# Kernel tuning notes

Hardware: AMD Instinct MI355X
Metric: run time of the kernel (lower is better)

Reference implementation:

```python
import jax, jax.numpy as jnp
import numpy as np

N_Q, N_T, D, C = 4096, 8192, 512, 16
SIGMA = 2.0


def setup_inputs() -> dict:
    key = jax.random.key(0)
    k1, k2, k3 = jax.random.split(key, 3)
    X = jax.random.normal(k1, (N_Q, D), dtype=jnp.float32)
    X_train = jax.random.normal(k2, (N_T, D), dtype=jnp.float32)
    y = jax.random.randint(k3, (N_T,), 0, C, dtype=jnp.int32)
    sigma = jnp.float32(SIGMA)
    return {"X": X, "X_train": X_train, "y": y, "sigma": sigma}


def reference(X, X_train, y, sigma):
    xx = jnp.sum(X * X, axis=1, keepdims=True)              # [N_q, 1]
    tt = jnp.sum(X_train * X_train, axis=1)                 # [N_t]
    cross = jnp.einsum('qd,td->qt', X, X_train)             # [N_q, N_t]
    dist2 = jnp.maximum(xx + tt[None, :] - 2.0 * cross, 0.0)
    pattern = jnp.exp(-dist2 / (2.0 * sigma ** 2))          # Gaussian RBF kernel [N_q, N_t]
    # per-class segment sum over training patterns (replaces per-class Python loop)
    summation = jax.ops.segment_sum(pattern.T, y, num_segments=C).T  # [N_q, C]
    summation = summation / jnp.sum(summation, axis=1, keepdims=True)
    return jnp.argmax(summation, axis=1)
```

## Files before the change

kernel.cpp:

```cpp
#include <hip/hip_runtime.h>


#define NQ 4096
#define NT 8192
#define DD 512
#define NC 16
#define LN_FLT_MIN -87.336544750402f
#define SCREEN_T 750.0f

typedef __attribute__((ext_vector_type(4))) int   v4i;
typedef __attribute__((ext_vector_type(8))) int   v8i;
typedef __attribute__((ext_vector_type(16))) float f32x16;

static __device__ __forceinline__ unsigned f2fp4(float x) {
  const float a = __builtin_fabsf(x);
  unsigned i = (unsigned)(a >= 0.25f) + (a >= 0.75f) + (a >= 1.25f)
             + (a >= 1.75f) + (a >= 2.5f) + (a >= 3.5f) + (a >= 5.0f);
  return i | (x < 0.0f ? 8u : 0u);
}

__global__ __launch_bounds__(256) void prep_k(const float* __restrict__ X,
                                              const float* __restrict__ XT,
                                              unsigned char* __restrict__ fXp,
                                              unsigned char* __restrict__ fTp,
                                              float* __restrict__ xx,
                                              float* __restrict__ tt,
                                              float* __restrict__ classacc) {
  const int lane = threadIdx.x & 63;
  const int row  = blockIdx.x * 4 + (threadIdx.x >> 6);
  const float* src; unsigned char* dst; float* nrm; int r;
  if (row < NT) { r = row; src = XT + (size_t)r * DD; dst = fTp; nrm = tt + r; }
  else { r = row - NT; src = X + (size_t)r * DD; dst = fXp; nrm = xx + r; }
  const float4* s4 = (const float4*)src;
  const float4 a = s4[lane * 2], b = s4[lane * 2 + 1];
  const unsigned word =  f2fp4(a.x)        | (f2fp4(a.y) << 4)
                      | (f2fp4(a.z) << 8)  | (f2fp4(a.w) << 12)
                      | (f2fp4(b.x) << 16) | (f2fp4(b.y) << 20)
                      | (f2fp4(b.z) << 24) | (f2fp4(b.w) << 28);
  const int l = (r & 31) + 32 * ((lane >> 2) & 1);
  const size_t dest = ((size_t)(r >> 5) * 8 + (lane >> 3)) * 1024
                    + l * 16 + (lane & 3) * 4;
  *(unsigned*)(dst + dest) = word;
  float acc = a.x*a.x + a.y*a.y + a.z*a.z + a.w*a.w
            + b.x*b.x + b.y*b.y + b.z*b.z + b.w*b.w;
  #pragma unroll
  for (int off = 32; off; off >>= 1) acc += __shfl_down(acc, off, 64);
  if (lane == 0) *nrm = acc;
  if (blockIdx.x < 64) {
    float4 z = {0.f, 0.f, 0.f, 0.f};
    ((float4*)classacc)[blockIdx.x * 256 + threadIdx.x] = z;
  }
}

#define MFMA4(A, B, C) __builtin_amdgcn_mfma_scale_f32_32x32x64_f8f6f4( \
    (A), (B), (C), 4, 4, 0, 127, 0, 127)
#define BAR() __builtin_amdgcn_s_barrier()
#define WAITV0() asm volatile("s_waitcnt vmcnt(0)" ::: "memory")
#define WAITLGKM0() asm volatile("s_waitcnt lgkmcnt(0)" ::: "memory")

static __device__ __forceinline__ void gll(const unsigned char* src, char* dst) {
  __builtin_amdgcn_global_load_lds(
      (const __attribute__((address_space(1))) unsigned int*)src,
      (__attribute__((address_space(3))) unsigned int*)dst, 16, 0, 0);
}

static __device__ __forceinline__ v8i pk8(v4i lo) {
  return __builtin_shufflevector(lo, lo, 0, 1, 2, 3, -1, -1, -1, -1);
}

__global__ __launch_bounds__(512, 1) void pnn_mfma(const unsigned char* __restrict__ fXp,
                                                   const unsigned char* __restrict__ fTp,
                                                   const float* __restrict__ Xf,
                                                   const float* __restrict__ Tf,
                                                   const int* __restrict__ y,
                                                   const float* __restrict__ sigp,
                                                   const float* __restrict__ xx,
                                                   const float* __restrict__ tt,
                                                   float* __restrict__ classacc) {
  extern __shared__ char lds[];
  float* const hxs = (float*)(lds + 131072);
  const int tid  = threadIdx.x;
  const int w    = tid >> 6, lane = tid & 63;
  const int la   = lane & 31, lb = lane >> 5;
  const int wr   = w >> 2, wc = w & 3;

  const int bid   = blockIdx.x;
  const int strip = bid & 7;
  const int qt    = bid >> 3;
  const int qbase = qt * 128;
  const int rt0   = (qbase >> 5) + wr * 2;

  const float sg = sigp[0];
  const float inv2s2 = 1.0f / (2.0f * sg * sg);

  v4i av[2][8];
  #pragma unroll
  for (int mt = 0; mt < 2; ++mt)
    #pragma unroll
    for (int kt = 0; kt < 8; ++kt)
      av[mt][kt] = *(const v4i*)(fXp + ((size_t)(rt0 + mt) * 8 + kt) * 1024 + lane * 16);

  if (tid < 128) hxs[tid] = (xx[qbase + tid] - SCREEN_T) * 0.5f;

#define STAGEB(buf, trt0) { \
    _Pragma("unroll") \
    for (int j = 0; j < 8; ++j) \
      gll(fTp + ((size_t)((trt0) + j) * 8 + w) * 1024 + lane * 16, \
          (buf) + (j * 8 + w) * 1024 + lane * 16); }

  char* cur = lds;
  char* nxt = lds + 65536;

  STAGEB(cur, strip * 32)
  WAITV0();
  WAITLGKM0();
  BAR();

  #pragma clang loop unroll(disable)
  for (int t = 0; t < 4; ++t) {
    if (t < 3) STAGEB(nxt, strip * 32 + (t + 1) * 8)

    f32x16 acc00 = (f32x16)(0.f), acc01 = (f32x16)(0.f);
    f32x16 acc10 = (f32x16)(0.f), acc11 = (f32x16)(0.f);

    #pragma unroll
    for (int kt = 0; kt < 8; ++kt) {
      const v4i b0 = *(const v4i*)(cur + ((wc * 2 + 0) * 8 + kt) * 1024 + lane * 16);
      const v4i b1 = *(const v4i*)(cur + ((wc * 2 + 1) * 8 + kt) * 1024 + lane * 16);
      const v8i a0 = pk8(av[0][kt]), a1 = pk8(av[1][kt]);
      const v8i bb0 = pk8(b0), bb1 = pk8(b1);
      acc00 = MFMA4(a0, bb0, acc00);
      acc01 = MFMA4(a0, bb1, acc01);
      acc10 = MFMA4(a1, bb0, acc10);
      acc11 = MFMA4(a1, bb1, acc11);
    }

    const int tbase = strip * 1024 + t * 256;
    const int wt = tbase + wc * 64;
    const float h0 = tt[wt + la] * 0.5f;
    const float h1 = tt[wt + 32 + la] * 0.5f;

#define EPIL(ACC, mt, HN, nt) { \
    _Pragma("unroll") \
    for (int reg = 0; reg < 16; ++reg) { \
      const int ql = wr * 64 + (mt) * 32 + (reg & 3) + 8 * (reg >> 2) + 4 * lb; \
      if (__builtin_expect((ACC)[reg] > hxs[ql] + (HN), 0)) { \
        const int q = qbase + ql; \
        const int tg = wt + (nt) * 32 + la; \
        const float4* xp = (const float4*)(Xf + (size_t)q * DD); \
        const float4* tp = (const float4*)(Tf + (size_t)tg * DD); \
        float s0 = 0.f, s1 = 0.f, s2 = 0.f, s3 = 0.f; \
        for (int d = 0; d < DD / 4; ++d) { \
          const float4 xv = xp[d], tv = tp[d]; \
          s0 = fmaf(xv.x, tv.x, s0); s1 = fmaf(xv.y, tv.y, s1); \
          s2 = fmaf(xv.z, tv.z, s2); s3 = fmaf(xv.w, tv.w, s3); \
        } \
        const float dot = (s0 + s1) + (s2 + s3); \
        const float dd2 = fmaxf(xx[q] + tt[tg] - 2.0f * dot, 0.f); \
        const float arg = -dd2 * inv2s2; \
        if (arg >= LN_FLT_MIN)             \
          atomicAdd(&classacc[q * NC + y[tg]], expf(arg)); \
      } \
    } }

    EPIL(acc00, 0, h0, 0)
    EPIL(acc01, 0, h1, 1)
    EPIL(acc10, 1, h0, 0)
    EPIL(acc11, 1, h1, 1)
#undef EPIL

    if (t < 3) {
      WAITV0();
      BAR();
      char* tmp = cur; cur = nxt; nxt = tmp;
    }
  }
#undef STAGEB
}

__global__ __launch_bounds__(256) void argmax_k(const float* __restrict__ classacc,
                                                float* __restrict__ out) {
  const int q = blockIdx.x * 256 + threadIdx.x;
  float sc[NC];
  #pragma unroll
  for (int c4 = 0; c4 < 4; ++c4) {
    const float4 v = ((const float4*)(classacc + (size_t)q * NC))[c4];
    sc[c4*4+0] = v.x; sc[c4*4+1] = v.y; sc[c4*4+2] = v.z; sc[c4*4+3] = v.w;
  }
  float rowsum = 0.f;
  #pragma unroll
  for (int c = 0; c < NC; ++c) rowsum += sc[c];
  int best = 0; float bv = sc[0];
  #pragma unroll
  for (int c = 1; c < NC; ++c)
    if (sc[c] > bv) { bv = sc[c]; best = c; }
  out[q] = (rowsum > 0.f) ? (float)best : 0.0f;
}

extern "C" void kernel_launch(void* const* d_in, const int* in_sizes, int n_in,
                              void* d_out, int out_size, void* d_ws, size_t ws_size,
                              hipStream_t stream) {
  const float* X  = (const float*)d_in[0];
  const float* XT = (const float*)d_in[1];
  const int*   y  = (const int*)d_in[2];
  const float* sg = (const float*)d_in[3];
  float* out = (float*)d_out;

  char* wsp = (char*)d_ws;
  unsigned char* fXp = (unsigned char*)wsp;
  unsigned char* fTp = fXp + (size_t)NQ * DD / 2;
  float* tt       = (float*)(wsp + 4u * 1024u * 1024u);
  float* xx       = tt + NT;
  float* classacc = xx + NQ;

  (void)hipFuncSetAttribute((const void*)pnn_mfma,
                            hipFuncAttributeMaxDynamicSharedMemorySize, 131584);

  prep_k<<<(NQ + NT) / 4, 256, 0, stream>>>(X, XT, fXp, fTp, xx, tt, classacc);
  pnn_mfma<<<256, 512, 131584, stream>>>(fXp, fTp, X, XT, y, sg, xx, tt, classacc);
  argmax_k<<<NQ / 256, 256, 0, stream>>>(classacc, out);
}
```

Before: 46.18 us.

## Load FP4 B tiles directly into registers instead of LDS double buffering

Removes the 128KB LDS double buffer and its global_load_lds staging, barriers and waits. Each wave now loads its own B fragments from global memory into registers and prefetches the next tile right after the MFMA loop. The epilogue first computes a per-lane max over the 16 accumulator entries, so the per-element screening branch is skipped in the common case. Dropping the large LDS allocation and the min-blocks launch bound could allow more blocks per CU. Waves in the same block no longer share staged data, so each fetches its own B data from global/L2 and register pressure rises.

Result: slower. 64.98 us (+40.7%).

```diff
diff --git a/kernel.cpp b/kernel.cpp
--- a/kernel.cpp
+++ b/kernel.cpp
@@ -54,31 +54,21 @@
 
 #define MFMA4(A, B, C) __builtin_amdgcn_mfma_scale_f32_32x32x64_f8f6f4( \
     (A), (B), (C), 4, 4, 0, 127, 0, 127)
-#define BAR() __builtin_amdgcn_s_barrier()
-#define WAITV0() asm volatile("s_waitcnt vmcnt(0)" ::: "memory")
-#define WAITLGKM0() asm volatile("s_waitcnt lgkmcnt(0)" ::: "memory")
-
-static __device__ __forceinline__ void gll(const unsigned char* src, char* dst) {
-  __builtin_amdgcn_global_load_lds(
-      (const __attribute__((address_space(1))) unsigned int*)src,
-      (__attribute__((address_space(3))) unsigned int*)dst, 16, 0, 0);
-}
 
 static __device__ __forceinline__ v8i pk8(v4i lo) {
   return __builtin_shufflevector(lo, lo, 0, 1, 2, 3, -1, -1, -1, -1);
 }
 
-__global__ __launch_bounds__(512, 1) void pnn_mfma(const unsigned char* __restrict__ fXp,
-                                                   const unsigned char* __restrict__ fTp,
-                                                   const float* __restrict__ Xf,
-                                                   const float* __restrict__ Tf,
-                                                   const int* __restrict__ y,
-                                                   const float* __restrict__ sigp,
-                                                   const float* __restrict__ xx,
-                                                   const float* __restrict__ tt,
-                                                   float* __restrict__ classacc) {
-  extern __shared__ char lds[];
-  float* const hxs = (float*)(lds + 131072);
+__global__ __launch_bounds__(512) void pnn_mfma(const unsigned char* __restrict__ fXp,
+                                                const unsigned char* __restrict__ fTp,
+                                                const float* __restrict__ Xf,
+                                                const float* __restrict__ Tf,
+                                                const int* __restrict__ y,
+                                                const float* __restrict__ sigp,
+                                                const float* __restrict__ xx,
+                                                const float* __restrict__ tt,
+                                                float* __restrict__ classacc) {
+  __shared__ float hxs[128];
   const int tid  = threadIdx.x;
   const int w    = tid >> 6, lane = tid & 63;
   const int la   = lane & 31, lb = lane >> 5;
@@ -88,7 +78,7 @@
   const int strip = bid & 7;
   const int qt    = bid >> 3;
   const int qbase = qt * 128;
-  const int rt0   = (qbase >> 5) + wr * 2;
+  const int art   = (qbase >> 5) + wr * 2;
 
   const float sg = sigp[0];
   const float inv2s2 = 1.0f / (2.0f * sg * sg);
@@ -98,84 +88,84 @@
   for (int mt = 0; mt < 2; ++mt)
     #pragma unroll
     for (int kt = 0; kt < 8; ++kt)
-      av[mt][kt] = *(const v4i*)(fXp + ((size_t)(rt0 + mt) * 8 + kt) * 1024 + lane * 16);
+      av[mt][kt] = *(const v4i*)(fXp + ((size_t)(art + mt) * 8 + kt) * 1024 + lane * 16);
 
   if (tid < 128) hxs[tid] = (xx[qbase + tid] - SCREEN_T) * 0.5f;
 
-#define STAGEB(buf, trt0) { \
-    _Pragma("unroll") \
-    for (int j = 0; j < 8; ++j) \
-      gll(fTp + ((size_t)((trt0) + j) * 8 + w) * 1024 + lane * 16, \
-          (buf) + (j * 8 + w) * 1024 + lane * 16); }
-
-  char* cur = lds;
-  char* nxt = lds + 65536;
-
-  STAGEB(cur, strip * 32)
-  WAITV0();
-  WAITLGKM0();
-  BAR();
+  v4i bv[2][8];
+  #pragma unroll
+  for (int j = 0; j < 2; ++j)
+    #pragma unroll
+    for (int kt = 0; kt < 8; ++kt)
+      bv[j][kt] = *(const v4i*)(fTp + ((size_t)(strip * 32 + wc * 2 + j) * 8 + kt) * 1024 + lane * 16);
+
+  __syncthreads();
 
   #pragma clang loop unroll(disable)
   for (int t = 0; t < 4; ++t) {
-    if (t < 3) STAGEB(nxt, strip * 32 + (t + 1) * 8)
+    const int tbase = strip * 1024 + t * 256;
+    const int wt = tbase + wc * 64;
+    const float hn0 = tt[wt + la] * 0.5f;
+    const float hn1 = tt[wt + 32 + la] * 0.5f;
 
     f32x16 acc00 = (f32x16)(0.f), acc01 = (f32x16)(0.f);
     f32x16 acc10 = (f32x16)(0.f), acc11 = (f32x16)(0.f);
 
     #pragma unroll
     for (int kt = 0; kt < 8; ++kt) {
-      const v4i b0 = *(const v4i*)(cur + ((wc * 2 + 0) * 8 + kt) * 1024 + lane * 16);
-      const v4i b1 = *(const v4i*)(cur + ((wc * 2 + 1) * 8 + kt) * 1024 + lane * 16);
       const v8i a0 = pk8(av[0][kt]), a1 = pk8(av[1][kt]);
-      const v8i bb0 = pk8(b0), bb1 = pk8(b1);
-      acc00 = MFMA4(a0, bb0, acc00);
-      acc01 = MFMA4(a0, bb1, acc01);
-      acc10 = MFMA4(a1, bb0, acc10);
-      acc11 = MFMA4(a1, bb1, acc11);
+      const v8i b0 = pk8(bv[0][kt]), b1 = pk8(bv[1][kt]);
+      acc00 = MFMA4(a0, b0, acc00);
+      acc01 = MFMA4(a0, b1, acc01);
+      acc10 = MFMA4(a1, b0, acc10);
+      acc11 = MFMA4(a1, b1, acc11);
     }
 
-    const int tbase = strip * 1024 + t * 256;
-    const int wt = tbase + wc * 64;
-    const float h0 = tt[wt + la] * 0.5f;
-    const float h1 = tt[wt + 32 + la] * 0.5f;
-
-#define EPIL(ACC, mt, HN, nt) { \
+    if (t < 3) {
+      #pragma unroll
+      for (int j = 0; j < 2; ++j)
+        #pragma unroll
+        for (int kt = 0; kt < 8; ++kt)
+          bv[j][kt] = *(const v4i*)(fTp + ((size_t)(strip * 32 + (t + 1) * 8 + wc * 2 + j) * 8 + kt) * 1024 + lane * 16);
+    }
+
+#define EPQ(ACC, mt, HN, nt) { \
+    float mx = -3.0e38f; \
     _Pragma("unroll") \
     for (int reg = 0; reg < 16; ++reg) { \
       const int ql = wr * 64 + (mt) * 32 + (reg & 3) + 8 * (reg >> 2) + 4 * lb; \
-      if (__builtin_expect((ACC)[reg] > hxs[ql] + (HN), 0)) { \
-        const int q = qbase + ql; \
-        const int tg = wt + (nt) * 32 + la; \
-        const float4* xp = (const float4*)(Xf + (size_t)q * DD); \
-        const float4* tp = (const float4*)(Tf + (size_t)tg * DD); \
-        float s0 = 0.f, s1 = 0.f, s2 = 0.f, s3 = 0.f; \
-        for (int d = 0; d < DD / 4; ++d) { \
-          const float4 xv = xp[d], tv = tp[d]; \
-          s0 = fmaf(xv.x, tv.x, s0); s1 = fmaf(xv.y, tv.y, s1); \
-          s2 = fmaf(xv.z, tv.z, s2); s3 = fmaf(xv.w, tv.w, s3); \
+      mx = fmaxf(mx, (ACC)[reg] - hxs[ql]); \
+    } \
+    if (__builtin_expect(mx > (HN), 0)) { \
+      _Pragma("unroll") \
+      for (int reg = 0; reg < 16; ++reg) { \
+        const int ql = wr * 64 + (mt) * 32 + (reg & 3) + 8 * (reg >> 2) + 4 * lb; \
+        if ((ACC)[reg] - hxs[ql] > (HN)) { \
+          const int q = qbase + ql; \
+          const int tg = wt + (nt) * 32 + la; \
+          const float4* xp = (const float4*)(Xf + (size_t)q * DD); \
+          const float4* tp = (const float4*)(Tf + (size_t)tg * DD); \
+          float s0 = 0.f, s1 = 0.f, s2 = 0.f, s3 = 0.f; \
+          for (int d = 0; d < DD / 4; ++d) { \
+            const float4 xv = xp[d], tv = tp[d]; \
+            s0 = fmaf(xv.x, tv.x, s0); s1 = fmaf(xv.y, tv.y, s1); \
+            s2 = fmaf(xv.z, tv.z, s2); s3 = fmaf(xv.w, tv.w, s3); \
+          } \
+          const float dot = (s0 + s1) + (s2 + s3); \
+          const float dd2 = fmaxf(xx[q] + tt[tg] - 2.0f * dot, 0.f); \
+          const float arg = -dd2 * inv2s2; \
+          if (arg >= LN_FLT_MIN)           \
+            atomicAdd(&classacc[q * NC + y[tg]], expf(arg)); \
         } \
-        const float dot = (s0 + s1) + (s2 + s3); \
-        const float dd2 = fmaxf(xx[q] + tt[tg] - 2.0f * dot, 0.f); \
-        const float arg = -dd2 * inv2s2; \
-        if (arg >= LN_FLT_MIN)             \
-          atomicAdd(&classacc[q * NC + y[tg]], expf(arg)); \
       } \
     } }
 
-    EPIL(acc00, 0, h0, 0)
-    EPIL(acc01, 0, h1, 1)
-    EPIL(acc10, 1, h0, 0)
-    EPIL(acc11, 1, h1, 1)
-#undef EPIL
-
-    if (t < 3) {
-      WAITV0();
-      BAR();
-      char* tmp = cur; cur = nxt; nxt = tmp;
-    }
+    EPQ(acc00, 0, hn0, 0)
+    EPQ(acc01, 0, hn1, 1)
+    EPQ(acc10, 1, hn0, 0)
+    EPQ(acc11, 1, hn1, 1)
+#undef EPQ
   }
-#undef STAGEB
 }
 
 __global__ __launch_bounds__(256) void argmax_k(const float* __restrict__ classacc,
@@ -213,10 +203,7 @@
   float* xx       = tt + NT;
   float* classacc = xx + NQ;
 
-  (void)hipFuncSetAttribute((const void*)pnn_mfma,
-                            hipFuncAttributeMaxDynamicSharedMemorySize, 131584);
-
   prep_k<<<(NQ + NT) / 4, 256, 0, stream>>>(X, XT, fXp, fTp, xx, tt, classacc);
-  pnn_mfma<<<256, 512, 131584, stream>>>(fXp, fTp, X, XT, y, sg, xx, tt, classacc);
+  pnn_mfma<<<256, 512, 0, stream>>>(fXp, fTp, X, XT, y, sg, xx, tt, classacc);
   argmax_k<<<NQ / 256, 256, 0, stream>>>(classacc, out);
 }
```

## Halve per-block train tile to launch twice as many blocks with smaller LDS

Applied to the files above, without the earlier changes.

Each block now covers 512 training points instead of 1024, using 16 strips per query tile, and the grid grows from 256 to 512 blocks. Each wave now holds one 32-wide N tile instead of two, and the LDS double buffer shrinks to 32KB per stage, so two blocks can share a CU. The launch bound no longer forces one block per SM. This is meant to raise occupancy and let one block's epilogue overlap with another block's MFMA work, on a device with 256 CUs. In exchange, each staged B tile is reused across less work, and the per-query A fragments are loaded twice as often across the grid.

Result: slower. 48.51 us (+5.0%).

```diff
diff --git a/kernel.cpp b/kernel.cpp
--- a/kernel.cpp
+++ b/kernel.cpp
@@ -56,7 +56,6 @@
     (A), (B), (C), 4, 4, 0, 127, 0, 127)
 #define BAR() __builtin_amdgcn_s_barrier()
 #define WAITV0() asm volatile("s_waitcnt vmcnt(0)" ::: "memory")
-#define WAITLGKM0() asm volatile("s_waitcnt lgkmcnt(0)" ::: "memory")
 
 static __device__ __forceinline__ void gll(const unsigned char* src, char* dst) {
   __builtin_amdgcn_global_load_lds(
@@ -68,30 +67,31 @@
   return __builtin_shufflevector(lo, lo, 0, 1, 2, 3, -1, -1, -1, -1);
 }
 
-__global__ __launch_bounds__(512, 1) void pnn_mfma(const unsigned char* __restrict__ fXp,
-                                                   const unsigned char* __restrict__ fTp,
-                                                   const float* __restrict__ Xf,
-                                                   const float* __restrict__ Tf,
-                                                   const int* __restrict__ y,
-                                                   const float* __restrict__ sigp,
-                                                   const float* __restrict__ xx,
-                                                   const float* __restrict__ tt,
-                                                   float* __restrict__ classacc) {
+__global__ __launch_bounds__(512) void pnn_mfma(const unsigned char* __restrict__ fXp,
+                                                const unsigned char* __restrict__ fTp,
+                                                const float* __restrict__ Xf,
+                                                const float* __restrict__ Tf,
+                                                const int* __restrict__ y,
+                                                const float* __restrict__ sigp,
+                                                const float* __restrict__ xx,
+                                                const float* __restrict__ tt,
+                                                float* __restrict__ classacc) {
   extern __shared__ char lds[];
-  float* const hxs = (float*)(lds + 131072);
+  float* const hxs = (float*)(lds + 65536);
   const int tid  = threadIdx.x;
   const int w    = tid >> 6, lane = tid & 63;
   const int la   = lane & 31, lb = lane >> 5;
   const int wr   = w >> 2, wc = w & 3;
 
   const int bid   = blockIdx.x;
-  const int strip = bid & 7;
-  const int qt    = bid >> 3;
+  const int strip = bid & 15;
+  const int qt    = bid >> 4;
   const int qbase = qt * 128;
   const int rt0   = (qbase >> 5) + wr * 2;
 
   const float sg = sigp[0];
   const float inv2s2 = 1.0f / (2.0f * sg * sg);
+  const int wq = qbase + wr * 64;
 
   v4i av[2][8];
   #pragma unroll
@@ -102,51 +102,43 @@
 
   if (tid < 128) hxs[tid] = (xx[qbase + tid] - SCREEN_T) * 0.5f;
 
-#define STAGEB(buf, trt0) { \
+#define STAGEB(buf, trt) { \
     _Pragma("unroll") \
-    for (int j = 0; j < 8; ++j) \
-      gll(fTp + ((size_t)((trt0) + j) * 8 + w) * 1024 + lane * 16, \
+    for (int j = 0; j < 4; ++j) \
+      gll(fTp + ((size_t)((trt) + j) * 8 + w) * 1024 + lane * 16, \
           (buf) + (j * 8 + w) * 1024 + lane * 16); }
 
   char* cur = lds;
-  char* nxt = lds + 65536;
-
-  STAGEB(cur, strip * 32)
-  WAITV0();
-  WAITLGKM0();
-  BAR();
+  char* nxt = lds + 32768;
+
+  STAGEB(cur, strip * 16)
+  __syncthreads();
 
   #pragma clang loop unroll(disable)
   for (int t = 0; t < 4; ++t) {
-    if (t < 3) STAGEB(nxt, strip * 32 + (t + 1) * 8)
-
-    f32x16 acc00 = (f32x16)(0.f), acc01 = (f32x16)(0.f);
-    f32x16 acc10 = (f32x16)(0.f), acc11 = (f32x16)(0.f);
+    if (t < 3) STAGEB(nxt, strip * 16 + (t + 1) * 4)
+
+    f32x16 acc0 = (f32x16)(0.f), acc1 = (f32x16)(0.f);
 
     #pragma unroll
     for (int kt = 0; kt < 8; ++kt) {
-      const v4i b0 = *(const v4i*)(cur + ((wc * 2 + 0) * 8 + kt) * 1024 + lane * 16);
-      const v4i b1 = *(const v4i*)(cur + ((wc * 2 + 1) * 8 + kt) * 1024 + lane * 16);
-      const v8i a0 = pk8(av[0][kt]), a1 = pk8(av[1][kt]);
-      const v8i bb0 = pk8(b0), bb1 = pk8(b1);
-      acc00 = MFMA4(a0, bb0, acc00);
-      acc01 = MFMA4(a0, bb1, acc01);
-      acc10 = MFMA4(a1, bb0, acc10);
-      acc11 = MFMA4(a1, bb1, acc11);
+      const v4i b = *(const v4i*)(cur + (wc * 8 + kt) * 1024 + lane * 16);
+      const v8i bb = pk8(b);
+      acc0 = MFMA4(pk8(av[0][kt]), bb, acc0);
+      acc1 = MFMA4(pk8(av[1][kt]), bb, acc1);
     }
 
-    const int tbase = strip * 1024 + t * 256;
-    const int wt = tbase + wc * 64;
-    const float h0 = tt[wt + la] * 0.5f;
-    const float h1 = tt[wt + 32 + la] * 0.5f;
-
-#define EPIL(ACC, mt, HN, nt) { \
+    const int tbase = strip * 512 + t * 128;
+    const int tg = tbase + wc * 32 + la;
+    const float tn = tt[tg] * 0.5f;
+    const int tc = y[tg];
+
+#define EPIL(ACC, mt) { \
     _Pragma("unroll") \
     for (int reg = 0; reg < 16; ++reg) { \
       const int ql = wr * 64 + (mt) * 32 + (reg & 3) + 8 * (reg >> 2) + 4 * lb; \
-      if (__builtin_expect((ACC)[reg] > hxs[ql] + (HN), 0)) { \
+      if (__builtin_expect((ACC)[reg] > hxs[ql] + tn, 0)) { \
         const int q = qbase + ql; \
-        const int tg = wt + (nt) * 32 + la; \
         const float4* xp = (const float4*)(Xf + (size_t)q * DD); \
         const float4* tp = (const float4*)(Tf + (size_t)tg * DD); \
         float s0 = 0.f, s1 = 0.f, s2 = 0.f, s3 = 0.f; \
@@ -159,21 +151,17 @@
         const float dd2 = fmaxf(xx[q] + tt[tg] - 2.0f * dot, 0.f); \
         const float arg = -dd2 * inv2s2; \
         if (arg >= LN_FLT_MIN)             \
-          atomicAdd(&classacc[q * NC + y[tg]], expf(arg)); \
+          atomicAdd(&classacc[q * NC + tc], expf(arg)); \
       } \
     } }
 
-    EPIL(acc00, 0, h0, 0)
-    EPIL(acc01, 0, h1, 1)
-    EPIL(acc10, 1, h0, 0)
-    EPIL(acc11, 1, h1, 1)
+    EPIL(acc0, 0)
+    EPIL(acc1, 1)
 #undef EPIL
 
-    if (t < 3) {
-      WAITV0();
-      BAR();
-      char* tmp = cur; cur = nxt; nxt = tmp;
-    }
+    WAITV0();
+    BAR();
+    char* tmp = cur; cur = nxt; nxt = tmp;
   }
 #undef STAGEB
 }
@@ -214,9 +202,9 @@
   float* classacc = xx + NQ;
 
   (void)hipFuncSetAttribute((const void*)pnn_mfma,
-                            hipFuncAttributeMaxDynamicSharedMemorySize, 131584);
+                            hipFuncAttributeMaxDynamicSharedMemorySize, 66048);
 
   prep_k<<<(NQ + NT) / 4, 256, 0, stream>>>(X, XT, fXp, fTp, xx, tt, classacc);
-  pnn_mfma<<<256, 512, 131584, stream>>>(fXp, fTp, X, XT, y, sg, xx, tt, classacc);
+  pnn_mfma<<<512, 512, 66048, stream>>>(fXp, fTp, X, XT, y, sg, xx, tt, classacc);
   argmax_k<<<NQ / 256, 256, 0, stream>>>(classacc, out);
 }
```
